# Performance work log

Hardware: AMD Instinct MI355X
Metric: run time of the kernel (lower is better)

Reference implementation:

```python
import jax, jax.numpy as jnp
import numpy as np

B, N, D = 2, 2048, 1024
H = 16
HD = D // H  # 64
SCALE = 8.0 / HD  # muP scale = 0.125
EPS = 1e-5


def setup_inputs() -> dict:
    key = jax.random.key(0)
    ks = jax.random.split(key, 7)
    s = 0.02  # realistic init scale for weights
    return {
        "xq": jax.random.normal(ks[0], (B, N, D), jnp.float32),
        "xk": jax.random.normal(ks[1], (B, N, D), jnp.float32),
        "xv": jax.random.normal(ks[2], (B, N, D), jnp.float32),
        "wq": jax.random.normal(ks[3], (D, D), jnp.float32) * s,
        "wk": jax.random.normal(ks[4], (D, D), jnp.float32) * s,
        "wv": jax.random.normal(ks[5], (D, D), jnp.float32) * s,
        "wproj": jax.random.normal(ks[6], (D, D), jnp.float32) * s,
    }


def _layernorm_noaffine(x):
    # Fp32LayerNorm over last dim, no bias / no affine params
    x32 = x.astype(jnp.float32)
    mu = jnp.mean(x32, axis=-1, keepdims=True)
    var = jnp.mean(jnp.square(x32 - mu), axis=-1, keepdims=True)
    return ((x32 - mu) * jax.lax.rsqrt(var + EPS)).astype(x.dtype)


def _heads(x):
    # [B, N, H*HD] -> [B, H, N, HD]
    b, n, _ = x.shape
    return x.reshape(b, n, H, HD).transpose(0, 2, 1, 3)


def reference(xq, xk, xv, wq, wk, wv, wproj):
    # nn.Linear: y = x @ W^T (no bias)
    q = _heads(xq @ wq.T)
    k = _heads(xk @ wk.T)
    v = _heads(xv @ wv.T)
    q = _layernorm_noaffine(q)
    k = _layernorm_noaffine(k)
    # dense attention (score_mod=None, block_mask=None), muP scale
    scores = jnp.einsum("bhqd,bhkd->bhqk", q, k) * SCALE
    attn = jax.nn.softmax(scores, axis=-1)
    o = jnp.einsum("bhqk,bhkd->bhqd", attn, v)
    o = o.transpose(0, 2, 1, 3).reshape(xq.shape[0], xq.shape[1], D)
    return o @ wproj.T
```

## Files before the change

### kernel.cpp

```cpp
#include <hip/hip_runtime.h>

typedef __bf16 bf16x8 __attribute__((ext_vector_type(8)));
typedef float f32x4 __attribute__((ext_vector_type(4)));
typedef float f32x16 __attribute__((ext_vector_type(16)));
typedef unsigned u32x4 __attribute__((ext_vector_type(4)));

#define DEV __device__ __forceinline__
#define L2E 1.44269504f

DEV unsigned short f2bf(float f) {
  unsigned u = __float_as_uint(f);
  u += 0x7fffu + ((u >> 16) & 1u);
  return (unsigned short)(u >> 16);
}
DEV float bf2f(unsigned short h) { return __uint_as_float(((unsigned)h) << 16); }

DEV void gload16(const void* g, void* l) {
  __builtin_amdgcn_global_load_lds((const __attribute__((address_space(1))) void*)g,
                                   (__attribute__((address_space(3))) void*)l, 16, 0, 0);
}

DEV unsigned cvtpk2(float lo, float hi) {
  unsigned r;
  asm("v_cvt_pk_bf16_f32 %0, %1, %2" : "=v"(r) : "v"(lo), "v"(hi));
  return r;
}
DEV void plswap(unsigned& a, unsigned& b) {
  asm volatile("v_permlane32_swap_b32 %0, %1" : "+v"(a), "+v"(b));
}
DEV float ex2(float x) {
  float r;
  asm("v_exp_f32 %0, %1" : "=v"(r) : "v"(x));
  return r;
}
DEV float max3(float a, float b, float c) {
  float r;
  asm("v_max3_f32 %0, %1, %2, %3" : "=v"(r) : "v"(a), "v"(b), "v"(c));
  return r;
}


__global__ __launch_bounds__(256) void cvt7(const float* xq, const float* xk, const float* xv,
                                            const float* wq, const float* wk, const float* wv,
                                            const float* wp, ushort4* xqb, ushort4* xkb,
                                            ushort4* xvb, ushort4* wqb, ushort4* wkb,
                                            ushort4* wvb, ushort4* wpb, int nx4, int nw4) {
  const int y = blockIdx.y;
  const float4* s;
  ushort4* d;
  int n;
  switch (y) {
    case 0: s = (const float4*)xq; d = xqb; n = nx4; break;
    case 1: s = (const float4*)xk; d = xkb; n = nx4; break;
    case 2: s = (const float4*)xv; d = xvb; n = nx4; break;
    case 3: s = (const float4*)wq; d = wqb; n = nw4; break;
    case 4: s = (const float4*)wk; d = wkb; n = nw4; break;
    case 5: s = (const float4*)wv; d = wvb; n = nw4; break;
    default: s = (const float4*)wp; d = wpb; n = nw4; break;
  }
  for (int i = blockIdx.x * 256 + threadIdx.x; i < n; i += gridDim.x * 256) {
    float4 v = s[i];
    ushort4 o;
    o.x = f2bf(v.x); o.y = f2bf(v.y); o.z = f2bf(v.z); o.w = f2bf(v.w);
    d[i] = o;
  }
}

template <bool SWAP>
DEV void gemm_core(const unsigned short* __restrict__ A, const unsigned short* __restrict__ W,
                   char* sA, char* sB, f32x4 acc[4][4], int bm, int bn, int tid) {
  const int w = tid >> 6, lane = tid & 63;
  const int wm = w >> 1, wn = w & 1;
  const char* aB = (const char*)A + ((size_t)(bm * 128 + (lane >> 3)) << 11) +
                   (((lane & 7) ^ (lane >> 3)) << 4);
  const char* bB = (const char*)W + ((size_t)(bn * 128 + (lane >> 3)) << 11) +
                   (((lane & 7) ^ (lane >> 3)) << 4);
  const int ldsBase = w * 1024;

  for (int kt = 0; kt < 16; ++kt) {
    const int ko = kt * 128;
#pragma unroll
    for (int c = 0; c < 4; ++c) {
      gload16(aB + ((size_t)(c * 32 + w * 8) << 11) + ko, sA + c * 4096 + ldsBase);
      gload16(bB + ((size_t)(c * 32 + w * 8) << 11) + ko, sB + c * 4096 + ldsBase);
    }
    __syncthreads();
#pragma unroll
    for (int kk = 0; kk < 2; ++kk) {
      const int ch = ((kk * 4 + (lane >> 4)) ^ (lane & 7)) << 4;
      bf16x8 aF[4], bF[4];
#pragma unroll
      for (int mi = 0; mi < 4; ++mi)
        aF[mi] = *(const bf16x8*)(sA + (wm * 64 + mi * 16 + (lane & 15)) * 128 + ch);
#pragma unroll
      for (int ni = 0; ni < 4; ++ni)
        bF[ni] = *(const bf16x8*)(sB + (wn * 64 + ni * 16 + (lane & 15)) * 128 + ch);
#pragma unroll
      for (int mi = 0; mi < 4; ++mi)
#pragma unroll
        for (int ni = 0; ni < 4; ++ni)
          acc[mi][ni] = SWAP ? __builtin_amdgcn_mfma_f32_16x16x32_bf16(bF[ni], aF[mi],
                                                                       acc[mi][ni], 0, 0, 0)
                             : __builtin_amdgcn_mfma_f32_16x16x32_bf16(aF[mi], bF[ni],
                                                                       acc[mi][ni], 0, 0, 0);
    }
    __syncthreads();
  }
}

__global__ __launch_bounds__(256, 3) void gemm_qkv(
    const unsigned short* __restrict__ xq, const unsigned short* __restrict__ xk,
    const unsigned short* __restrict__ xv, const unsigned short* __restrict__ wq,
    const unsigned short* __restrict__ wk, const unsigned short* __restrict__ wv,
    unsigned short* __restrict__ qh, unsigned short* __restrict__ kh,
    unsigned short* __restrict__ vt) {
  __shared__ char sA[16384], sB[16384];
  const int z = blockIdx.z;
  const int flat = blockIdx.x + (blockIdx.y << 3);
  const int xcd = flat & 7, ii = flat >> 3;
  const int bm = xcd * 4 + (ii >> 3), bn = ii & 7;
  const int tid = threadIdx.x, w = tid >> 6, lane = tid & 63;
  const int wm = w >> 1, wn = w & 1;

  if (z == 2) {
    f32x4 acc[4][4];
#pragma unroll
    for (int i = 0; i < 4; ++i)
#pragma unroll
      for (int j = 0; j < 4; ++j) acc[i][j] = (f32x4){0.f, 0.f, 0.f, 0.f};
    gemm_core<false>(xv, wv, sA, sB, acc, bm, bn, tid);
    const int hb = bn * 2 + wn;
    const int d = (lane & 15);
    const int g0 = bm * 128 + wm * 64 + ((lane >> 4) << 2);
#pragma unroll
    for (int mi = 0; mi < 4; ++mi) {
      const int g = g0 + mi * 16;
      const int b = g >> 11, n0 = g & 2047, tq = n0 >> 6, nn = n0 & 63;
#pragma unroll
      for (int ni = 0; ni < 4; ++ni) {
        const int dd = d + ni * 16;
        char* dst = (char*)vt + ((size_t)((b * 16 + hb) * 32 + tq) << 13) +
                    (((nn >> 4) * 2 + (dd >> 5)) << 10) + (((nn >> 3) & 1) << 9) +
                    ((dd & 31) << 4) + ((nn & 7) << 1);
        *(uint2*)dst = make_uint2(cvtpk2(acc[mi][ni][0], acc[mi][ni][1]),
                                  cvtpk2(acc[mi][ni][2], acc[mi][ni][3]));
      }
    }
  } else {
    const unsigned short* A = z == 0 ? xq : xk;
    const unsigned short* W = z == 0 ? wq : wk;
    f32x4 acc[4][4];
#pragma unroll
    for (int i = 0; i < 4; ++i)
#pragma unroll
      for (int j = 0; j < 4; ++j) acc[i][j] = (f32x4){0.f, 0.f, 0.f, 0.f};
    gemm_core<true>(A, W, sA, sB, acc, bm, bn, tid);
    unsigned short* dst = z == 0 ? qh : kh;
    const float osc = z == 0 ? 0.125f * L2E : 1.0f;
    const int h = bn * 2 + wn;
    const int hiK = lane >> 5;
    const int low8 = ((lane >> 4) & 1) << 3;
#pragma unroll
    for (int mi = 0; mi < 4; ++mi) {
      float s = 0.f, ss = 0.f;
#pragma unroll
      for (int ni = 0; ni < 4; ++ni)
#pragma unroll
        for (int r = 0; r < 4; ++r) {
          const float v = acc[mi][ni][r];
          s += v;
          ss += v * v;
        }
      s += __shfl_xor(s, 16); ss += __shfl_xor(ss, 16);
      s += __shfl_xor(s, 32); ss += __shfl_xor(ss, 32);
      const float mean = s * 0.015625f;
      const float var = ss * 0.015625f - mean * mean;
      const float rstd = rsqrtf(var + 1e-5f) * osc;
      const float mr = mean * rstd;
      const int g = bm * 128 + wm * 64 + mi * 16 + (lane & 15);
      const int b = g >> 11, n = g & 2047;
      const int bh = b * 16 + h, tq = n >> 6, rr = n & 63;
      char* tbase = (char*)dst + ((size_t)(bh * 32 + tq) << 13);
#pragma unroll
      for (int ni = 0; ni < 4; ++ni) {
        const unsigned u0 = cvtpk2(fmaf(acc[mi][ni][0], rstd, -mr), fmaf(acc[mi][ni][1], rstd, -mr));
        const unsigned u1 = cvtpk2(fmaf(acc[mi][ni][2], rstd, -mr), fmaf(acc[mi][ni][3], rstd, -mr));
        char* p = tbase + ((ni * 2 + (rr >> 5)) << 10) + (hiK << 9) + ((rr & 31) << 4) + low8;
        *(uint2*)p = make_uint2(u0, u1);
      }
    }
  }
}

__global__ __launch_bounds__(256, 3) void gemm_out(const unsigned short* __restrict__ A,
                                                   const unsigned short* __restrict__ Wp,
                                                   float* __restrict__ C) {
  __shared__ char sA[16384], sB[8192];
  const int flat = blockIdx.x + (blockIdx.y << 4);
  const int xcd = flat & 7, ii = flat >> 3;
  const int bm = xcd * 4 + (ii & 3), bn = ii >> 2;
  const int tid = threadIdx.x, w = tid >> 6, lane = tid & 63;
  const int wm = w >> 1, wn = w & 1;
  f32x4 acc[4][2];
#pragma unroll
  for (int i = 0; i < 4; ++i)
#pragma unroll
    for (int j = 0; j < 2; ++j) acc[i][j] = (f32x4){0.f, 0.f, 0.f, 0.f};

  const char* aB = (const char*)A + ((size_t)(bm * 128 + (lane >> 3)) << 11) +
                   (((lane & 7) ^ (lane >> 3)) << 4);
  const char* bB = (const char*)Wp + ((size_t)(bn * 64 + (lane >> 3)) << 11) +
                   (((lane & 7) ^ (lane >> 3)) << 4);
  const int ldsBase = w * 1024;
  for (int kt = 0; kt < 16; ++kt) {
    const int ko = kt * 128;
#pragma unroll
    for (int c = 0; c < 4; ++c)
      gload16(aB + ((size_t)(c * 32 + w * 8) << 11) + ko, sA + c * 4096 + ldsBase);
#pragma unroll
    for (int c = 0; c < 2; ++c)
      gload16(bB + ((size_t)(c * 32 + w * 8) << 11) + ko, sB + c * 4096 + ldsBase);
    __syncthreads();
#pragma unroll
    for (int kk = 0; kk < 2; ++kk) {
      const int ch = ((kk * 4 + (lane >> 4)) ^ (lane & 7)) << 4;
      bf16x8 aF[4], bF[2];
#pragma unroll
      for (int mi = 0; mi < 4; ++mi)
        aF[mi] = *(const bf16x8*)(sA + (wm * 64 + mi * 16 + (lane & 15)) * 128 + ch);
#pragma unroll
      for (int ni = 0; ni < 2; ++ni)
        bF[ni] = *(const bf16x8*)(sB + (wn * 32 + ni * 16 + (lane & 15)) * 128 + ch);
#pragma unroll
      for (int mi = 0; mi < 4; ++mi)
#pragma unroll
        for (int ni = 0; ni < 2; ++ni)
          acc[mi][ni] = __builtin_amdgcn_mfma_f32_16x16x32_bf16(bF[ni], aF[mi], acc[mi][ni], 0, 0, 0);
    }
    __syncthreads();
  }
  const int m0 = bm * 128 + wm * 64 + (lane & 15);
  const int nb = bn * 64 + wn * 32 + ((lane >> 4) << 2);
#pragma unroll
  for (int mi = 0; mi < 4; ++mi)
#pragma unroll
    for (int ni = 0; ni < 2; ++ni) {
      const f32x4 v = acc[mi][ni];
      *(float4*)&C[(size_t)(m0 + mi * 16) * 1024 + nb + ni * 16] =
          make_float4(v[0], v[1], v[2], v[3]);
    }
}

__global__ __launch_bounds__(256, 3) void attn_fused(
    const unsigned short* __restrict__ Qp, const unsigned short* __restrict__ Kp,
    const unsigned short* __restrict__ Vp, unsigned short* __restrict__ Opart,
    float2* __restrict__ ML) {
  const int bid = blockIdx.x;
  const int xcd = bid & 7, idx = bid >> 3;
  const int bh = ((idx & 3) << 3) | xcd;
  const int rest = idx >> 2;
  const int half = rest & 1;
  const int qt = rest >> 1;
  __shared__ char smem[49152];
  const int tid = threadIdx.x, w = tid >> 6, lane = tid & 63;
  const int q5 = lane & 31, hi = lane >> 5;

  const char* qg = (const char*)Qp + ((size_t)(bh * 32 + qt * 2) << 13);
  const char* kg = (const char*)Kp + ((size_t)(bh * 32 + half * 16) << 13);
  const char* vg = (const char*)Vp + ((size_t)(bh * 32 + half * 16) << 13);

#pragma unroll
  for (int t = 0; t < 4; ++t)
    gload16(qg + (w * 4 + t) * 1024 + lane * 16, smem + (w * 4 + t) * 1024);
  __syncthreads();
  bf16x8 qf[4];
  {
    const int qbase = (w >> 1) * 8192 + ((w & 1) << 10);
#pragma unroll
    for (int dc = 0; dc < 4; ++dc)
      qf[dc] = *(const bf16x8*)(smem + qbase + (dc << 11) + lane * 16);
  }
  __syncthreads();

#pragma unroll
  for (int tt = 0; tt < 2; ++tt)
#pragma unroll
    for (int t = 0; t < 2; ++t) {
      gload16(kg + (size_t)tt * 8192 + (w * 2 + t) * 1024 + lane * 16,
              smem + tt * 8192 + (w * 2 + t) * 1024);
      gload16(vg + (size_t)tt * 8192 + (w * 2 + t) * 1024 + lane * 16,
              smem + 24576 + tt * 8192 + (w * 2 + t) * 1024);
    }

  const u32x4 onesw = {0x3F803F80u, 0x3F803F80u, 0x3F803F80u, 0x3F803F80u};
  const bf16x8 ones = __builtin_bit_cast(bf16x8, onesw);

  f32x16 o0 = {0,0,0,0,0,0,0,0,0,0,0,0,0,0,0,0};
  f32x16 o1 = {0,0,0,0,0,0,0,0,0,0,0,0,0,0,0,0};
  f32x16 lacc = {0,0,0,0,0,0,0,0,0,0,0,0,0,0,0,0};
  float m = -1e30f;

#define ATTN_TILE(kOff, vOff)                                                     \
  {                                                                               \
    f32x16 s0 = {0,0,0,0,0,0,0,0,0,0,0,0,0,0,0,0};                                \
    f32x16 s1 = {0,0,0,0,0,0,0,0,0,0,0,0,0,0,0,0};                                \
    __builtin_amdgcn_s_setprio(1);                                                \
    _Pragma("unroll") for (int dc = 0; dc < 4; ++dc) {                            \
      const bf16x8 kf0 = *(const bf16x8*)(smem + (kOff) + (dc << 11) + lane * 16);\
      const bf16x8 kf1 =                                                          \
          *(const bf16x8*)(smem + (kOff) + (dc << 11) + 1024 + lane * 16);        \
      s0 = __builtin_amdgcn_mfma_f32_32x32x16_bf16(kf0, qf[dc], s0, 0, 0, 0);     \
      s1 = __builtin_amdgcn_mfma_f32_32x32x16_bf16(kf1, qf[dc], s1, 0, 0, 0);     \
    }                                                                             \
    __builtin_amdgcn_s_setprio(0);                                                \
    float tt[12];                                                                 \
    _Pragma("unroll") for (int r = 0; r < 10; ++r) {                              \
      const float a = (3 * r) < 16 ? s0[(3 * r) & 15] : s1[(3 * r) & 15];         \
      const float b = (3 * r + 1) < 16 ? s0[(3 * r + 1) & 15] : s1[(3 * r + 1) & 15]; \
      const float c = (3 * r + 2) < 16 ? s0[(3 * r + 2) & 15] : s1[(3 * r + 2) & 15]; \
      tt[r] = max3(a, b, c);                                                      \
    }                                                                             \
    tt[10] = s1[14]; tt[11] = s1[15];                                             \
    tt[0] = max3(tt[0], tt[1], tt[2]);                                            \
    tt[1] = max3(tt[3], tt[4], tt[5]);                                            \
    tt[2] = max3(tt[6], tt[7], tt[8]);                                            \
    tt[3] = max3(tt[9], tt[10], tt[11]);                                          \
    const float loc = fmaxf(max3(tt[0], tt[1], tt[2]), tt[3]);                    \
    const float mx = fmaxf(loc, __shfl_xor(loc, 32));                             \
    if (__any(mx > m + 8.f)) {                                                    \
      const float mn = fmaxf(m, mx);                                              \
      const float corr = ex2(m - mn);                                             \
      lacc[0] *= corr;                                                            \
      _Pragma("unroll") for (int r = 0; r < 16; ++r) { o0[r] *= corr; o1[r] *= corr; } \
      m = mn;                                                                     \
    }                                                                             \
    const float nm = -m;                                                          \
    unsigned pk[4][4];                                                            \
    DO_CHUNK(0, s0, 0)                                                            \
    DO_CHUNK(1, s0, 8)                                                            \
    DO_CHUNK(2, s1, 0)                                                            \
    DO_CHUNK(3, s1, 8)                                                            \
    __builtin_amdgcn_s_setprio(1);                                                \
    _Pragma("unroll") for (int kk = 0; kk < 4; ++kk) {                            \
      const bf16x8 vf0 = *(const bf16x8*)(smem + (vOff) + (kk << 11) + lane * 16);\
      const bf16x8 vf1 =                                                          \
          *(const bf16x8*)(smem + (vOff) + (kk << 11) + 1024 + lane * 16);        \
      const u32x4 pw = {pk[kk][0], pk[kk][1], pk[kk][2], pk[kk][3]};              \
      const bf16x8 pb = __builtin_bit_cast(bf16x8, pw);                           \
      o0 = __builtin_amdgcn_mfma_f32_32x32x16_bf16(vf0, pb, o0, 0, 0, 0);         \
      o1 = __builtin_amdgcn_mfma_f32_32x32x16_bf16(vf1, pb, o1, 0, 0, 0);         \
      lacc = __builtin_amdgcn_mfma_f32_32x32x16_bf16(ones, pb, lacc, 0, 0, 0);    \
    }                                                                             \
    __builtin_amdgcn_s_setprio(0);                                                \
  }

#define DO_CHUNK(c, SV, B)                                      \
  {                                                             \
    float p0 = ex2(SV[B + 0] + nm);                             \
    float p1 = ex2(SV[B + 1] + nm);                             \
    float p2 = ex2(SV[B + 2] + nm);                             \
    float p3 = ex2(SV[B + 3] + nm);                             \
    float p4 = ex2(SV[B + 4] + nm);                             \
    float p5 = ex2(SV[B + 5] + nm);                             \
    float p6 = ex2(SV[B + 6] + nm);                             \
    float p7 = ex2(SV[B + 7] + nm);                             \
    unsigned a0 = cvtpk2(p0, p1), a1 = cvtpk2(p2, p3);          \
    unsigned b0 = cvtpk2(p4, p5), b1 = cvtpk2(p6, p7);          \
    plswap(a0, b0);                                             \
    plswap(a1, b1);                                             \
    pk[c][0] = a0; pk[c][1] = a1; pk[c][2] = b0; pk[c][3] = b1; \
  }

  int cb = 0;
  for (int kt = 0; kt < 15; ++kt) {
    asm volatile("s_waitcnt vmcnt(4)" ::: "memory");
    __builtin_amdgcn_s_barrier();
    __builtin_amdgcn_sched_barrier(0);
    if (kt < 14) {
      const int pb = cb == 0 ? 2 : cb - 1;
      const char* kgp = kg + ((size_t)(kt + 2) << 13);
      const char* vgp = vg + ((size_t)(kt + 2) << 13);
#pragma unroll
      for (int t = 0; t < 2; ++t) {
        gload16(kgp + (w * 2 + t) * 1024 + lane * 16, smem + pb * 8192 + (w * 2 + t) * 1024);
        gload16(vgp + (w * 2 + t) * 1024 + lane * 16,
                smem + 24576 + pb * 8192 + (w * 2 + t) * 1024);
      }
    }
    const int kOff = cb * 8192, vOff = 24576 + cb * 8192;
    ATTN_TILE(kOff, vOff)
    cb = cb == 2 ? 0 : cb + 1;
  }
  {
    asm volatile("s_waitcnt vmcnt(0)" ::: "memory");
    __builtin_amdgcn_s_barrier();
    __builtin_amdgcn_sched_barrier(0);
    const int kOff = cb * 8192, vOff = 24576 + cb * 8192;
    ATTN_TILE(kOff, vOff)
  }
#undef DO_CHUNK
#undef ATTN_TILE

  const float l = lacc[0];
  const float invl = 1.f / l;
  const int q = qt * 128 + w * 32 + q5;
  const size_t prow = (size_t)(half * 32 + bh) * 2048 + q;
  unsigned short* ob = Opart + prow * 64;
#pragma unroll
  for (int g = 0; g < 4; ++g) {
    unsigned d0 = cvtpk2(o0[4 * g + 0] * invl, o0[4 * g + 1] * invl);
    unsigned d1 = cvtpk2(o0[4 * g + 2] * invl, o0[4 * g + 3] * invl);
    *(uint2*)(ob + 8 * g + 4 * hi) = make_uint2(d0, d1);
    unsigned e0 = cvtpk2(o1[4 * g + 0] * invl, o1[4 * g + 1] * invl);
    unsigned e1 = cvtpk2(o1[4 * g + 2] * invl, o1[4 * g + 3] * invl);
    *(uint2*)(ob + 32 + 8 * g + 4 * hi) = make_uint2(e0, e1);
  }
  if (hi == 0) ML[prow] = make_float2(m, l);
}

__global__ __launch_bounds__(256) void attn_merge(const unsigned short* __restrict__ Op,
                                                  const float2* __restrict__ ML,
                                                  unsigned short* __restrict__ O) {
  const int gid = blockIdx.x * 256 + threadIdx.x;
  const int row = gid >> 3, sub = gid & 7;
  float2 ml[2];
  float mm = -1e30f;
#pragma unroll
  for (int p = 0; p < 2; ++p) {
    ml[p] = ML[p * 65536 + row];
    mm = fmaxf(mm, ml[p].x);
  }
  float wgt[2], wsum = 0.f;
#pragma unroll
  for (int p = 0; p < 2; ++p) {
    wgt[p] = ml[p].y * ex2(ml[p].x - mm);
    wsum += wgt[p];
  }
  const float inv = 1.f / wsum;
  float r[8] = {0.f, 0.f, 0.f, 0.f, 0.f, 0.f, 0.f, 0.f};
#pragma unroll
  for (int p = 0; p < 2; ++p) {
    const uint4 a = *(const uint4*)(Op + ((size_t)(p * 65536) + row) * 64 + sub * 8);
    const unsigned av[4] = {a.x, a.y, a.z, a.w};
#pragma unroll
    for (int j = 0; j < 4; ++j) {
      r[2 * j] += wgt[p] * bf2f((unsigned short)(av[j] & 0xffff));
      r[2 * j + 1] += wgt[p] * bf2f((unsigned short)(av[j] >> 16));
    }
  }
  unsigned ov[4];
#pragma unroll
  for (int j = 0; j < 4; ++j)
    ov[j] = cvtpk2(r[2 * j] * inv, r[2 * j + 1] * inv);
  const int bh = row >> 11, q = row & 2047, bb = bh >> 4, h = bh & 15;
  *(uint4*)(O + ((size_t)(bb * 2048 + q) * 1024 + h * 64 + sub * 8)) =
      make_uint4(ov[0], ov[1], ov[2], ov[3]);
}

extern "C" void kernel_launch(void* const* d_in, const int* in_sizes, int n_in,
                              void* d_out, int out_size, void* d_ws, size_t ws_size,
                              hipStream_t stream) {
  const float* xq = (const float*)d_in[0];
  const float* xk = (const float*)d_in[1];
  const float* xv = (const float*)d_in[2];
  const float* wq = (const float*)d_in[3];
  const float* wk = (const float*)d_in[4];
  const float* wv = (const float*)d_in[5];
  const float* wp = (const float*)d_in[6];

  const size_t NX = 4194304;
  const size_t NW = 1048576;
  unsigned short* base = (unsigned short*)d_ws;
  unsigned short* xqb = base;
  unsigned short* xkb = base + NX;
  unsigned short* xvb = base + 2 * NX;
  unsigned short* wqb = base + 3 * NX;
  unsigned short* wkb = wqb + NW;
  unsigned short* wvb = wkb + NW;
  unsigned short* wpb = base + 3 * NX + 4 * NW;
  unsigned short* qh = wpb + NW;
  unsigned short* kh = qh + NX;
  unsigned short* vt = kh + NX;
  unsigned short* obf = vt + NX;
  float2* ml = (float2*)(obf + NX);
  unsigned short* opart = base;

  cvt7<<<dim3(512, 7), 256, 0, stream>>>(xq, xk, xv, wq, wk, wv, wp, (ushort4*)xqb,
                                         (ushort4*)xkb, (ushort4*)xvb, (ushort4*)wqb,
                                         (ushort4*)wkb, (ushort4*)wvb, (ushort4*)wpb,
                                         (int)(NX / 4), (int)(NW / 4));

  gemm_qkv<<<dim3(8, 32, 3), 256, 0, stream>>>(xqb, xkb, xvb, wqb, wkb, wvb, qh, kh, vt);

  attn_fused<<<1024, 256, 0, stream>>>(qh, kh, vt, opart, ml);
  attn_merge<<<2048, 256, 0, stream>>>(opart, ml, obf);

  gemm_out<<<dim3(16, 32), 256, 0, stream>>>(obf, wpb, (float*)d_out);
}
```

Before: 126.1 us.

## Software-pipeline QK^T of next tile with softmax and PV of current tile

Restructures the attention loop into a two-stage ping-pong: the QK^T MFMAs for the next key tile are issued before the softmax and PV work of the current tile, using separate K and V LDS slots. Shared memory shrinks from three K/V buffer pairs to two K plus two V buffers. The row sum is now accumulated in scalar registers with a cross-half shuffle, replacing the extra ones-matrix MFMA per PV step. The trade-off is that each barrier now waits for all outstanding loads, so the earlier two-deep prefetch is gone and global load latency may be less hidden.

```diff
diff --git a/kernel.cpp b/kernel.cpp
--- a/kernel.cpp
+++ b/kernel.cpp
@@ -261,7 +261,7 @@
   const int rest = idx >> 2;
   const int half = rest & 1;
   const int qt = rest >> 1;
-  __shared__ char smem[49152];
+  __shared__ char smem[32768];
   const int tid = threadIdx.x, w = tid >> 6, lane = tid & 63;
   const int q5 = lane & 31, hi = lane >> 5;
 
@@ -282,78 +282,30 @@
   }
   __syncthreads();
 
-#pragma unroll
-  for (int tt = 0; tt < 2; ++tt)
-#pragma unroll
-    for (int t = 0; t < 2; ++t) {
-      gload16(kg + (size_t)tt * 8192 + (w * 2 + t) * 1024 + lane * 16,
-              smem + tt * 8192 + (w * 2 + t) * 1024);
-      gload16(vg + (size_t)tt * 8192 + (w * 2 + t) * 1024 + lane * 16,
-              smem + 24576 + tt * 8192 + (w * 2 + t) * 1024);
-    }
-
-  const u32x4 onesw = {0x3F803F80u, 0x3F803F80u, 0x3F803F80u, 0x3F803F80u};
-  const bf16x8 ones = __builtin_bit_cast(bf16x8, onesw);
-
-  f32x16 o0 = {0,0,0,0,0,0,0,0,0,0,0,0,0,0,0,0};
-  f32x16 o1 = {0,0,0,0,0,0,0,0,0,0,0,0,0,0,0,0};
-  f32x16 lacc = {0,0,0,0,0,0,0,0,0,0,0,0,0,0,0,0};
-  float m = -1e30f;
-
-#define ATTN_TILE(kOff, vOff)                                                     \
+#define STGK(T, OFF)                                                              \
   {                                                                               \
-    f32x16 s0 = {0,0,0,0,0,0,0,0,0,0,0,0,0,0,0,0};                                \
-    f32x16 s1 = {0,0,0,0,0,0,0,0,0,0,0,0,0,0,0,0};                                \
-    __builtin_amdgcn_s_setprio(1);                                                \
+    _Pragma("unroll") for (int t_ = 0; t_ < 2; ++t_)                              \
+        gload16(kg + ((size_t)(T) << 13) + (w * 2 + t_) * 1024 + lane * 16,       \
+                smem + (OFF) + (w * 2 + t_) * 1024);                              \
+  }
+#define STGV(T, OFF)                                                              \
+  {                                                                               \
+    _Pragma("unroll") for (int t_ = 0; t_ < 2; ++t_)                              \
+        gload16(vg + ((size_t)(T) << 13) + (w * 2 + t_) * 1024 + lane * 16,       \
+                smem + (OFF) + (w * 2 + t_) * 1024);                              \
+  }
+#define QKT(kOff, S0v, S1v)                                                       \
+  {                                                                               \
+    S0v = (f32x16){0,0,0,0,0,0,0,0,0,0,0,0,0,0,0,0};                              \
+    S1v = (f32x16){0,0,0,0,0,0,0,0,0,0,0,0,0,0,0,0};                              \
     _Pragma("unroll") for (int dc = 0; dc < 4; ++dc) {                            \
       const bf16x8 kf0 = *(const bf16x8*)(smem + (kOff) + (dc << 11) + lane * 16);\
       const bf16x8 kf1 =                                                          \
           *(const bf16x8*)(smem + (kOff) + (dc << 11) + 1024 + lane * 16);        \
-      s0 = __builtin_amdgcn_mfma_f32_32x32x16_bf16(kf0, qf[dc], s0, 0, 0, 0);     \
-      s1 = __builtin_amdgcn_mfma_f32_32x32x16_bf16(kf1, qf[dc], s1, 0, 0, 0);     \
+      S0v = __builtin_amdgcn_mfma_f32_32x32x16_bf16(kf0, qf[dc], S0v, 0, 0, 0);   \
+      S1v = __builtin_amdgcn_mfma_f32_32x32x16_bf16(kf1, qf[dc], S1v, 0, 0, 0);   \
     }                                                                             \
-    __builtin_amdgcn_s_setprio(0);                                                \
-    float tt[12];                                                                 \
-    _Pragma("unroll") for (int r = 0; r < 10; ++r) {                              \
-      const float a = (3 * r) < 16 ? s0[(3 * r) & 15] : s1[(3 * r) & 15];         \
-      const float b = (3 * r + 1) < 16 ? s0[(3 * r + 1) & 15] : s1[(3 * r + 1) & 15]; \
-      const float c = (3 * r + 2) < 16 ? s0[(3 * r + 2) & 15] : s1[(3 * r + 2) & 15]; \
-      tt[r] = max3(a, b, c);                                                      \
-    }                                                                             \
-    tt[10] = s1[14]; tt[11] = s1[15];                                             \
-    tt[0] = max3(tt[0], tt[1], tt[2]);                                            \
-    tt[1] = max3(tt[3], tt[4], tt[5]);                                            \
-    tt[2] = max3(tt[6], tt[7], tt[8]);                                            \
-    tt[3] = max3(tt[9], tt[10], tt[11]);                                          \
-    const float loc = fmaxf(max3(tt[0], tt[1], tt[2]), tt[3]);                    \
-    const float mx = fmaxf(loc, __shfl_xor(loc, 32));                             \
-    if (__any(mx > m + 8.f)) {                                                    \
-      const float mn = fmaxf(m, mx);                                              \
-      const float corr = ex2(m - mn);                                             \
-      lacc[0] *= corr;                                                            \
-      _Pragma("unroll") for (int r = 0; r < 16; ++r) { o0[r] *= corr; o1[r] *= corr; } \
-      m = mn;                                                                     \
-    }                                                                             \
-    const float nm = -m;                                                          \
-    unsigned pk[4][4];                                                            \
-    DO_CHUNK(0, s0, 0)                                                            \
-    DO_CHUNK(1, s0, 8)                                                            \
-    DO_CHUNK(2, s1, 0)                                                            \
-    DO_CHUNK(3, s1, 8)                                                            \
-    __builtin_amdgcn_s_setprio(1);                                                \
-    _Pragma("unroll") for (int kk = 0; kk < 4; ++kk) {                            \
-      const bf16x8 vf0 = *(const bf16x8*)(smem + (vOff) + (kk << 11) + lane * 16);\
-      const bf16x8 vf1 =                                                          \
-          *(const bf16x8*)(smem + (vOff) + (kk << 11) + 1024 + lane * 16);        \
-      const u32x4 pw = {pk[kk][0], pk[kk][1], pk[kk][2], pk[kk][3]};              \
-      const bf16x8 pb = __builtin_bit_cast(bf16x8, pw);                           \
-      o0 = __builtin_amdgcn_mfma_f32_32x32x16_bf16(vf0, pb, o0, 0, 0, 0);         \
-      o1 = __builtin_amdgcn_mfma_f32_32x32x16_bf16(vf1, pb, o1, 0, 0, 0);         \
-      lacc = __builtin_amdgcn_mfma_f32_32x32x16_bf16(ones, pb, lacc, 0, 0, 0);    \
-    }                                                                             \
-    __builtin_amdgcn_s_setprio(0);                                                \
-  }
-
+  }
 #define DO_CHUNK(c, SV, B)                                      \
   {                                                             \
     float p0 = ex2(SV[B + 0] + nm);                             \
@@ -364,44 +316,90 @@
     float p5 = ex2(SV[B + 5] + nm);                             \
     float p6 = ex2(SV[B + 6] + nm);                             \
     float p7 = ex2(SV[B + 7] + nm);                             \
+    rs += ((p0 + p1) + (p2 + p3)) + ((p4 + p5) + (p6 + p7));    \
     unsigned a0 = cvtpk2(p0, p1), a1 = cvtpk2(p2, p3);          \
     unsigned b0 = cvtpk2(p4, p5), b1 = cvtpk2(p6, p7);          \
     plswap(a0, b0);                                             \
     plswap(a1, b1);                                             \
     pk[c][0] = a0; pk[c][1] = a1; pk[c][2] = b0; pk[c][3] = b1; \
   }
-
-  int cb = 0;
-  for (int kt = 0; kt < 15; ++kt) {
-    asm volatile("s_waitcnt vmcnt(4)" ::: "memory");
-    __builtin_amdgcn_s_barrier();
-    __builtin_amdgcn_sched_barrier(0);
-    if (kt < 14) {
-      const int pb = cb == 0 ? 2 : cb - 1;
-      const char* kgp = kg + ((size_t)(kt + 2) << 13);
-      const char* vgp = vg + ((size_t)(kt + 2) << 13);
-#pragma unroll
-      for (int t = 0; t < 2; ++t) {
-        gload16(kgp + (w * 2 + t) * 1024 + lane * 16, smem + pb * 8192 + (w * 2 + t) * 1024);
-        gload16(vgp + (w * 2 + t) * 1024 + lane * 16,
-                smem + 24576 + pb * 8192 + (w * 2 + t) * 1024);
-      }
-    }
-    const int kOff = cb * 8192, vOff = 24576 + cb * 8192;
-    ATTN_TILE(kOff, vOff)
-    cb = cb == 2 ? 0 : cb + 1;
-  }
-  {
-    asm volatile("s_waitcnt vmcnt(0)" ::: "memory");
-    __builtin_amdgcn_s_barrier();
-    __builtin_amdgcn_sched_barrier(0);
-    const int kOff = cb * 8192, vOff = 24576 + cb * 8192;
-    ATTN_TILE(kOff, vOff)
-  }
+#define SOFTPV(S0v, S1v, vOff)                                                    \
+  {                                                                               \
+    float tt[12];                                                                 \
+    _Pragma("unroll") for (int r = 0; r < 10; ++r) {                              \
+      const float a = (3 * r) < 16 ? S0v[(3 * r) & 15] : S1v[(3 * r) & 15];       \
+      const float b = (3 * r + 1) < 16 ? S0v[(3 * r + 1) & 15] : S1v[(3 * r + 1) & 15]; \
+      const float c = (3 * r + 2) < 16 ? S0v[(3 * r + 2) & 15] : S1v[(3 * r + 2) & 15]; \
+      tt[r] = max3(a, b, c);                                                      \
+    }                                                                             \
+    tt[10] = S1v[14]; tt[11] = S1v[15];                                           \
+    tt[0] = max3(tt[0], tt[1], tt[2]);                                            \
+    tt[1] = max3(tt[3], tt[4], tt[5]);                                            \
+    tt[2] = max3(tt[6], tt[7], tt[8]);                                            \
+    tt[3] = max3(tt[9], tt[10], tt[11]);                                          \
+    const float loc = fmaxf(max3(tt[0], tt[1], tt[2]), tt[3]);                    \
+    const float mx = fmaxf(loc, __shfl_xor(loc, 32));                             \
+    if (__any(mx > m + 8.f)) {                                                    \
+      const float mn = fmaxf(m, mx);                                              \
+      const float corr = ex2(m - mn);                                             \
+      l *= corr;                                                                  \
+      _Pragma("unroll") for (int r = 0; r < 16; ++r) { o0[r] *= corr; o1[r] *= corr; } \
+      m = mn;                                                                     \
+    }                                                                             \
+    const float nm = -m;                                                          \
+    float rs = 0.f;                                                               \
+    unsigned pk[4][4];                                                            \
+    DO_CHUNK(0, S0v, 0)                                                           \
+    DO_CHUNK(1, S0v, 8)                                                           \
+    DO_CHUNK(2, S1v, 0)                                                           \
+    DO_CHUNK(3, S1v, 8)                                                           \
+    rs += __shfl_xor(rs, 32);                                                     \
+    l += rs;                                                                      \
+    __builtin_amdgcn_s_setprio(1);                                                \
+    _Pragma("unroll") for (int kk = 0; kk < 4; ++kk) {                            \
+      const bf16x8 vf0 = *(const bf16x8*)(smem + (vOff) + (kk << 11) + lane * 16);\
+      const bf16x8 vf1 =                                                          \
+          *(const bf16x8*)(smem + (vOff) + (kk << 11) + 1024 + lane * 16);        \
+      const u32x4 pw = {pk[kk][0], pk[kk][1], pk[kk][2], pk[kk][3]};              \
+      const bf16x8 pb = __builtin_bit_cast(bf16x8, pw);                           \
+      o0 = __builtin_amdgcn_mfma_f32_32x32x16_bf16(vf0, pb, o0, 0, 0, 0);         \
+      o1 = __builtin_amdgcn_mfma_f32_32x32x16_bf16(vf1, pb, o1, 0, 0, 0);         \
+    }                                                                             \
+    __builtin_amdgcn_s_setprio(0);                                                \
+  }
+
+  STGK(0, 0)
+  STGK(1, 8192)
+  STGV(0, 16384)
+  __syncthreads();
+
+  f32x16 o0 = {0,0,0,0,0,0,0,0,0,0,0,0,0,0,0,0};
+  f32x16 o1 = {0,0,0,0,0,0,0,0,0,0,0,0,0,0,0,0};
+  f32x16 sA0, sA1, sB0, sB1;
+  float m = -1e30f, l = 0.f;
+
+  QKT(0, sA0, sA1)
+
+  for (int tp = 0; tp < 8; ++tp) {
+    __syncthreads();
+    if (tp < 7) STGK(2 * tp + 2, 0)
+    STGV(2 * tp + 1, 24576)
+    QKT(8192, sB0, sB1)
+    SOFTPV(sA0, sA1, 16384)
+    __syncthreads();
+    if (tp < 7) {
+      STGK(2 * tp + 3, 8192)
+      STGV(2 * tp + 2, 16384)
+      QKT(0, sA0, sA1)
+    }
+    SOFTPV(sB0, sB1, 24576)
+  }
+#undef STGK
+#undef STGV
+#undef QKT
 #undef DO_CHUNK
-#undef ATTN_TILE
-
-  const float l = lacc[0];
+#undef SOFTPV
+
   const float invl = 1.f / l;
   const int q = qt * 128 + w * 32 + q5;
   const size_t prow = (size_t)(half * 32 + bh) * 2048 + q;
```

New measurement: 124.6 us. No clear change (-1.2%).
